# Optimization experiments

Measured on AMD Instinct MI355X. Metric: run time of the kernel, lower is better.

## Reference

```python
import jax, jax.numpy as jnp
import numpy as np

H = 16  # num_heads

def setup_inputs() -> dict:
    key = jax.random.key(0)
    k1, k2, k3, k4 = jax.random.split(key, 4)
    B, N, E = 2, 2048, 2048
    return {
        "hidden_states": jax.random.normal(k1, (B, N, E), jnp.float32),
        "w_fused": jax.random.normal(k2, (E, 3 * E), jnp.float32) * (E ** -0.5),
        "w_proj": jax.random.normal(k3, (E, E), jnp.float32) * (E ** -0.5),
        "b_proj": jax.random.normal(k4, (E,), jnp.float32),
    }

def reference(hidden_states, w_fused, w_proj, b_proj):
    B, N, E = hidden_states.shape
    D = E // H  # head_dim
    qkv = hidden_states @ w_fused                      # [B,N,3E]
    q, k, v = jnp.split(qkv, 3, axis=-1)               # each [B,N,E]
    def to_heads(t):
        return t.reshape(B, N, H, D).transpose(0, 2, 1, 3)  # [B,H,N,D]
    q, k, v = to_heads(q), to_heads(k), to_heads(v)
    scores = jnp.einsum('bhnd,bhmd->bhnm', q, k) / jnp.asarray(D ** 0.5, q.dtype)
    causal = jnp.tril(jnp.ones((N, N), dtype=bool))    # [N,N]
    mask_value = jnp.asarray(jnp.finfo(scores.dtype).min, scores.dtype)
    scores = jnp.where(causal[None, None], scores, mask_value)
    attn_weights = jax.nn.softmax(scores, axis=-1)     # [B,H,N,N]
    attn_out = jnp.einsum('bhnm,bhmd->bhnd', attn_weights, v)
    attn_out = attn_out.transpose(0, 2, 1, 3).reshape(B, N, E)  # b n (h d)
    out = attn_out @ w_proj + b_proj
    return out, attn_weights
```

## Files before the change

### kernel.cpp

```cpp
#include <hip/hip_runtime.h>
#include <hip/hip_bf16.h>

typedef __attribute__((ext_vector_type(4))) float f32x4;
typedef __attribute__((ext_vector_type(8))) __bf16 bf16x8;


__device__ inline unsigned short f2bf(float f) {
  union { float f; unsigned u; } x; x.f = f;
  unsigned r = x.u + 0x7fffu + ((x.u >> 16) & 1u);
  return (unsigned short)(r >> 16);
}

__device__ inline void stage_bf16_tile(const ushort* __restrict__ g, int ldg, ushort* l) {
  int tid = threadIdx.x;
#pragma unroll
  for (int t = 0; t < 4; ++t) {
    int c = tid + t * 256;
    int m = c >> 3, kc = (c & 7) << 3;
    *(int4*)(l + m * 72 + kc) = *(const int4*)(g + (size_t)m * ldg + kc);
  }
}

__device__ inline void stage_f32_tile(const float* __restrict__ g, int ldg, ushort* l) {
  int tid = threadIdx.x;
#pragma unroll
  for (int t = 0; t < 8; ++t) {
    int c = tid + t * 256;
    int m = c >> 4, kc = (c & 15) << 2;
    float4 v = *(const float4*)(g + (size_t)m * ldg + kc);
    ushort4 o; o.x = f2bf(v.x); o.y = f2bf(v.y); o.z = f2bf(v.z); o.w = f2bf(v.w);
    *(ushort4*)(l + m * 72 + kc) = o;
  }
}

__device__ inline void mma_tile(const ushort* lA, const ushort* lB, f32x4 acc[4][4]) {
  int lane = threadIdx.x & 63, w = threadIdx.x >> 6;
  int wm = (w & 1) << 6, wn = (w >> 1) << 6;
  int row = lane & 15, quad = lane >> 4;
#pragma unroll
  for (int kk = 0; kk < 64; kk += 32) {
    bf16x8 a[4], b[4];
#pragma unroll
    for (int i = 0; i < 4; ++i)
      a[i] = *(const bf16x8*)(lA + (wm + i * 16 + row) * 72 + kk + quad * 8);
#pragma unroll
    for (int j = 0; j < 4; ++j)
      b[j] = *(const bf16x8*)(lB + (wn + j * 16 + row) * 72 + kk + quad * 8);
#pragma unroll
    for (int i = 0; i < 4; ++i)
#pragma unroll
      for (int j = 0; j < 4; ++j)
        acc[i][j] = __builtin_amdgcn_mfma_f32_16x16x32_bf16(a[i], b[j], acc[i][j], 0, 0, 0);
  }
}


__global__ __launch_bounds__(256) void k_cvt_bf16(const float* __restrict__ in,
                                                  ushort* __restrict__ out, int n4) {
  int i = blockIdx.x * 256 + threadIdx.x;
  if (i >= n4) return;
  float4 v = *(const float4*)(in + (size_t)i * 4);
  ushort4 o; o.x = f2bf(v.x); o.y = f2bf(v.y); o.z = f2bf(v.z); o.w = f2bf(v.w);
  *(ushort4*)(out + (size_t)i * 4) = o;
}

__global__ __launch_bounds__(256) void k_transpose_bf16(const float* __restrict__ in,
                                                        ushort* __restrict__ out, int R, int C) {
  __shared__ __align__(16) ushort t[64][72];
  int c0 = blockIdx.x << 6, r0 = blockIdx.y << 6;
  int tid = threadIdx.x;
#pragma unroll
  for (int it = 0; it < 4; ++it) {
    int idx = tid + it * 256;
    int r = idx >> 4, c4 = (idx & 15) << 2;
    float4 v = *(const float4*)(in + (size_t)(r0 + r) * C + c0 + c4);
    t[c4][r] = f2bf(v.x); t[c4 + 1][r] = f2bf(v.y);
    t[c4 + 2][r] = f2bf(v.z); t[c4 + 3][r] = f2bf(v.w);
  }
  __syncthreads();
#pragma unroll
  for (int it = 0; it < 4; ++it) {
    int idx = tid + it * 256;
    int c = idx >> 4, r4 = (idx & 15) << 2;
    ushort4 o; o.x = t[c][r4]; o.y = t[c][r4 + 1]; o.z = t[c][r4 + 2]; o.w = t[c][r4 + 3];
    *(ushort4*)(out + (size_t)(c0 + c) * R + r0 + r4) = o;
  }
}

__global__ __launch_bounds__(256) void k_qkv(const ushort* __restrict__ A,
                                             const ushort* __restrict__ Bt,
                                             ushort* __restrict__ qh,
                                             ushort* __restrict__ kh,
                                             ushort* __restrict__ vt) {
  __shared__ __align__(16) ushort lA[128 * 72];
  __shared__ __align__(16) ushort lB[128 * 72];
  int rt = blockIdx.x, ct = blockIdx.y;
  f32x4 z = {0.f, 0.f, 0.f, 0.f};
  f32x4 acc[4][4];
#pragma unroll
  for (int i = 0; i < 4; ++i)
#pragma unroll
    for (int j = 0; j < 4; ++j) acc[i][j] = z;
  for (int kt = 0; kt < 2048; kt += 64) {
    __syncthreads();
    stage_bf16_tile(A + (size_t)rt * 128 * 2048 + kt, 2048, lA);
    stage_bf16_tile(Bt + (size_t)ct * 128 * 2048 + kt, 2048, lB);
    __syncthreads();
    mma_tile(lA, lB, acc);
  }
  int lane = threadIdx.x & 63, w = threadIdx.x >> 6;
  int wm = (w & 1) << 6, wn = (w >> 1) << 6;
  int col = lane & 15, rb = (lane >> 4) << 2;
#pragma unroll
  for (int i = 0; i < 4; ++i)
#pragma unroll
    for (int j = 0; j < 4; ++j)
#pragma unroll
      for (int r = 0; r < 4; ++r) {
        int R = rt * 128 + wm + i * 16 + rb + r;
        int C = ct * 128 + wn + j * 16 + col;
        int b = R >> 11, n = R & 2047;
        int seg = C >> 11, hh = (C >> 7) & 15, d = C & 127;
        int bh = b * 16 + hh;
        float v = acc[i][j][r];
        if (seg == 0)      qh[((size_t)bh * 2048 + n) * 128 + d] = f2bf(v * 0.08838834764831845f);
        else if (seg == 1) kh[((size_t)bh * 2048 + n) * 128 + d] = f2bf(v);
        else               vt[((size_t)bh * 128 + d) * 2048 + n] = f2bf(v);
      }
}

__global__ __launch_bounds__(256) void k_scores(const ushort* __restrict__ qh,
                                                const ushort* __restrict__ kh,
                                                float* __restrict__ sc) {
  int rt = blockIdx.x, ct = blockIdx.y, bh = blockIdx.z;
  if (ct > rt) return;
  __shared__ __align__(16) ushort lA[128 * 72];
  __shared__ __align__(16) ushort lB[128 * 72];
  f32x4 z = {0.f, 0.f, 0.f, 0.f};
  f32x4 acc[4][4];
#pragma unroll
  for (int i = 0; i < 4; ++i)
#pragma unroll
    for (int j = 0; j < 4; ++j) acc[i][j] = z;
  const ushort* Ab = qh + (size_t)bh * 2048 * 128 + (size_t)rt * 128 * 128;
  const ushort* Bb = kh + (size_t)bh * 2048 * 128 + (size_t)ct * 128 * 128;
#pragma unroll
  for (int kt = 0; kt < 128; kt += 64) {
    __syncthreads();
    stage_bf16_tile(Ab + kt, 128, lA);
    stage_bf16_tile(Bb + kt, 128, lB);
    __syncthreads();
    mma_tile(lA, lB, acc);
  }
  float* base = sc + (size_t)bh * 2048 * 2048;
  int lane = threadIdx.x & 63, w = threadIdx.x >> 6;
  int wm = (w & 1) << 6, wn = (w >> 1) << 6;
  int col = lane & 15, rb = (lane >> 4) << 2;
#pragma unroll
  for (int i = 0; i < 4; ++i)
#pragma unroll
    for (int j = 0; j < 4; ++j)
#pragma unroll
      for (int r = 0; r < 4; ++r) {
        int R = rt * 128 + wm + i * 16 + rb + r;
        int C = ct * 128 + wn + j * 16 + col;
        base[(size_t)R * 2048 + C] = acc[i][j][r];
      }
}

__global__ __launch_bounds__(256) void k_softmax(float* __restrict__ sc) {
  int row = blockIdx.x;
  int n = row & 2047;
  float* p = sc + (size_t)row * 2048;
  int tid = threadIdx.x;
  float vals[8];
  float mx = -INFINITY;
#pragma unroll
  for (int t = 0; t < 2; ++t) {
    float4 v = *(const float4*)(p + t * 1024 + tid * 4);
    float vv[4] = {v.x, v.y, v.z, v.w};
#pragma unroll
    for (int i = 0; i < 4; ++i) {
      int m = t * 1024 + tid * 4 + i;
      float x = (m <= n) ? vv[i] : -INFINITY;
      vals[t * 4 + i] = x;
      mx = fmaxf(mx, x);
    }
  }
#pragma unroll
  for (int o = 32; o > 0; o >>= 1) mx = fmaxf(mx, __shfl_xor(mx, o));
  __shared__ float red[4];
  if ((tid & 63) == 0) red[tid >> 6] = mx;
  __syncthreads();
  mx = fmaxf(fmaxf(red[0], red[1]), fmaxf(red[2], red[3]));
  float s = 0.f;
#pragma unroll
  for (int e = 0; e < 8; ++e) { float ev = expf(vals[e] - mx); vals[e] = ev; s += ev; }
#pragma unroll
  for (int o = 32; o > 0; o >>= 1) s += __shfl_xor(s, o);
  __syncthreads();
  if ((tid & 63) == 0) red[tid >> 6] = s;
  __syncthreads();
  float inv = 1.f / (red[0] + red[1] + red[2] + red[3]);
#pragma unroll
  for (int t = 0; t < 2; ++t) {
    float4 v;
    v.x = vals[t * 4 + 0] * inv; v.y = vals[t * 4 + 1] * inv;
    v.z = vals[t * 4 + 2] * inv; v.w = vals[t * 4 + 3] * inv;
    *(float4*)(p + t * 1024 + tid * 4) = v;
  }
}

__global__ __launch_bounds__(256) void k_pv(const float* __restrict__ sc,
                                            const ushort* __restrict__ vt,
                                            ushort* __restrict__ Ao) {
  int rt = blockIdx.x, bh = blockIdx.y;
  __shared__ __align__(16) ushort lA[128 * 72];
  __shared__ __align__(16) ushort lB[128 * 72];
  f32x4 z = {0.f, 0.f, 0.f, 0.f};
  f32x4 acc[4][4];
#pragma unroll
  for (int i = 0; i < 4; ++i)
#pragma unroll
    for (int j = 0; j < 4; ++j) acc[i][j] = z;
  const float* Pb = sc + (size_t)bh * 2048 * 2048 + (size_t)rt * 128 * 2048;
  const ushort* Vb = vt + (size_t)bh * 128 * 2048;
  int kend = (rt + 1) * 128;
  for (int kt = 0; kt < kend; kt += 64) {
    __syncthreads();
    stage_f32_tile(Pb + kt, 2048, lA);
    stage_bf16_tile(Vb + kt, 2048, lB);
    __syncthreads();
    mma_tile(lA, lB, acc);
  }
  int b = bh >> 4, hh = bh & 15;
  int lane = threadIdx.x & 63, w = threadIdx.x >> 6;
  int wm = (w & 1) << 6, wn = (w >> 1) << 6;
  int col = lane & 15, rb = (lane >> 4) << 2;
#pragma unroll
  for (int i = 0; i < 4; ++i)
#pragma unroll
    for (int j = 0; j < 4; ++j)
#pragma unroll
      for (int r = 0; r < 4; ++r) {
        int R = rt * 128 + wm + i * 16 + rb + r;
        int C = wn + j * 16 + col;
        Ao[((size_t)b * 2048 + R) * 2048 + hh * 128 + C] = f2bf(acc[i][j][r]);
      }
}

__global__ __launch_bounds__(256) void k_proj(const ushort* __restrict__ Ao,
                                              const ushort* __restrict__ Wt,
                                              const float* __restrict__ bias,
                                              float* __restrict__ out) {
  int rt = blockIdx.x, ct = blockIdx.y;
  __shared__ __align__(16) ushort lA[128 * 72];
  __shared__ __align__(16) ushort lB[128 * 72];
  f32x4 z = {0.f, 0.f, 0.f, 0.f};
  f32x4 acc[4][4];
#pragma unroll
  for (int i = 0; i < 4; ++i)
#pragma unroll
    for (int j = 0; j < 4; ++j) acc[i][j] = z;
  for (int kt = 0; kt < 2048; kt += 64) {
    __syncthreads();
    stage_bf16_tile(Ao + (size_t)rt * 128 * 2048 + kt, 2048, lA);
    stage_bf16_tile(Wt + (size_t)ct * 128 * 2048 + kt, 2048, lB);
    __syncthreads();
    mma_tile(lA, lB, acc);
  }
  int lane = threadIdx.x & 63, w = threadIdx.x >> 6;
  int wm = (w & 1) << 6, wn = (w >> 1) << 6;
  int col = lane & 15, rb = (lane >> 4) << 2;
#pragma unroll
  for (int i = 0; i < 4; ++i)
#pragma unroll
    for (int j = 0; j < 4; ++j)
#pragma unroll
      for (int r = 0; r < 4; ++r) {
        int R = rt * 128 + wm + i * 16 + rb + r;
        int C = ct * 128 + wn + j * 16 + col;
        out[(size_t)R * 2048 + C] = acc[i][j][r] + bias[C];
      }
}


extern "C" void kernel_launch(void* const* d_in, const int* in_sizes, int n_in,
                              void* d_out, int out_size, void* d_ws, size_t ws_size,
                              hipStream_t stream) {
  const float* hs = (const float*)d_in[0];
  const float* wf = (const float*)d_in[1];
  const float* wp = (const float*)d_in[2];
  const float* bp = (const float*)d_in[3];
  float* out = (float*)d_out;
  float* attnw = out + (size_t)8388608;

  ushort* Hb  = (ushort*)d_ws;
  ushort* Wft = Hb  + (size_t)8388608;
  ushort* Wpt = Wft + (size_t)12582912;
  ushort* qh  = Wpt + (size_t)4194304;
  ushort* kh  = qh  + (size_t)8388608;
  ushort* vt  = kh  + (size_t)8388608;
  ushort* Ao  = vt  + (size_t)8388608;

  k_cvt_bf16<<<8192, 256, 0, stream>>>(hs, Hb, 2097152);
  k_transpose_bf16<<<dim3(96, 32), 256, 0, stream>>>(wf, Wft, 2048, 6144);
  k_transpose_bf16<<<dim3(32, 32), 256, 0, stream>>>(wp, Wpt, 2048, 2048);
  k_qkv<<<dim3(32, 48), 256, 0, stream>>>(Hb, Wft, qh, kh, vt);
  k_scores<<<dim3(16, 16, 32), 256, 0, stream>>>(qh, kh, attnw);
  k_softmax<<<65536, 256, 0, stream>>>(attnw);
  k_pv<<<dim3(16, 32), 256, 0, stream>>>(attnw, vt, Ao);
  k_proj<<<dim3(32, 16), 256, 0, stream>>>(Ao, Wpt, bp, out);
}
```

Baseline: 1.140 ms.

## Fuse scores, softmax and PV into a two-pass causal attention kernel

Replaces the separate scores, softmax and PV kernels with one kernel per (head, row-tile). The first pass computes QK^T tiles to build the online row max and sum. The second pass recomputes the scores, writes the normalized probabilities to the attention-weights output, and multiplies them by V from LDS. The upper triangle is zero-filled directly, and row tiles are interleaved to balance the causal work. This removes the fp32 score write/read/rewrite round trips and the read of P by the PV stage, at the cost of computing QK^T twice and adding extra block-wide syncs.

```diff
diff --git a/kernel.cpp b/kernel.cpp
--- a/kernel.cpp
+++ b/kernel.cpp
@@ -21,18 +21,6 @@
   }
 }
 
-__device__ inline void stage_f32_tile(const float* __restrict__ g, int ldg, ushort* l) {
-  int tid = threadIdx.x;
-#pragma unroll
-  for (int t = 0; t < 8; ++t) {
-    int c = tid + t * 256;
-    int m = c >> 4, kc = (c & 15) << 2;
-    float4 v = *(const float4*)(g + (size_t)m * ldg + kc);
-    ushort4 o; o.x = f2bf(v.x); o.y = f2bf(v.y); o.z = f2bf(v.z); o.w = f2bf(v.w);
-    *(ushort4*)(l + m * 72 + kc) = o;
-  }
-}
-
 __device__ inline void mma_tile(const ushort* lA, const ushort* lB, f32x4 acc[4][4]) {
   int lane = threadIdx.x & 63, w = threadIdx.x >> 6;
   int wm = (w & 1) << 6, wn = (w >> 1) << 6;
@@ -46,6 +34,27 @@
 #pragma unroll
     for (int j = 0; j < 4; ++j)
       b[j] = *(const bf16x8*)(lB + (wn + j * 16 + row) * 72 + kk + quad * 8);
+#pragma unroll
+    for (int i = 0; i < 4; ++i)
+#pragma unroll
+      for (int j = 0; j < 4; ++j)
+        acc[i][j] = __builtin_amdgcn_mfma_f32_16x16x32_bf16(a[i], b[j], acc[i][j], 0, 0, 0);
+  }
+}
+
+__device__ inline void mma_pv(const ushort* lP, const ushort* lV, int kk2, f32x4 acc[4][4]) {
+  int lane = threadIdx.x & 63, w = threadIdx.x >> 6;
+  int wm = (w & 1) << 6, wn = (w >> 1) << 6;
+  int row = lane & 15, quad = lane >> 4;
+#pragma unroll
+  for (int kk = 0; kk < 64; kk += 32) {
+    bf16x8 a[4], b[4];
+#pragma unroll
+    for (int i = 0; i < 4; ++i)
+      a[i] = *(const bf16x8*)(lP + (wm + i * 16 + row) * 136 + kk2 * 64 + kk + quad * 8);
+#pragma unroll
+    for (int j = 0; j < 4; ++j)
+      b[j] = *(const bf16x8*)(lV + (wn + j * 16 + row) * 72 + kk + quad * 8);
 #pragma unroll
     for (int i = 0; i < 4; ++i)
 #pragma unroll
@@ -129,123 +138,169 @@
       }
 }
 
-__global__ __launch_bounds__(256) void k_scores(const ushort* __restrict__ qh,
-                                                const ushort* __restrict__ kh,
-                                                float* __restrict__ sc) {
-  int rt = blockIdx.x, ct = blockIdx.y, bh = blockIdx.z;
-  if (ct > rt) return;
-  __shared__ __align__(16) ushort lA[128 * 72];
-  __shared__ __align__(16) ushort lB[128 * 72];
+__global__ __launch_bounds__(256, 2) void k_attn(const ushort* __restrict__ qh,
+                                                 const ushort* __restrict__ kh,
+                                                 const ushort* __restrict__ vt,
+                                                 float* __restrict__ attnw,
+                                                 ushort* __restrict__ Ao) {
+  __shared__ __align__(16) ushort lAB[2 * 128 * 72];
+  __shared__ __align__(16) ushort lV[128 * 72];
+  __shared__ float mArr[128], lArr[128], invA[128], tm0[128], tm1[128];
+
+  int id = blockIdx.x;
+  int r5 = id & 31, p = r5 >> 1;
+  int rt = (r5 & 1) ? p : 15 - p;
+  int bh = ((id >> 5) << 1) | ((id >> 4) & 1);
+
+  ushort* lA = lAB;
+  ushort* lB = lAB + 128 * 72;
+  int tid = threadIdx.x;
+  int lane = tid & 63, w = tid >> 6;
+  int wm = (w & 1) << 6, wn = (w >> 1) << 6;
+  int c16 = lane & 15, quad = lane >> 4;
+
+  const ushort* Qb = qh + ((size_t)bh * 2048 + rt * 128) * 128;
+  const ushort* Kb = kh + (size_t)bh * 2048 * 128;
+  const ushort* Vb = vt + (size_t)bh * 128 * 2048;
+  float* Pg = attnw + (size_t)bh * 2048 * 2048 + (size_t)rt * 128 * 2048;
+
+  if (tid < 128) { mArr[tid] = -INFINITY; lArr[tid] = 0.f; }
+  __syncthreads();
+
   f32x4 z = {0.f, 0.f, 0.f, 0.f};
-  f32x4 acc[4][4];
-#pragma unroll
-  for (int i = 0; i < 4; ++i)
-#pragma unroll
-    for (int j = 0; j < 4; ++j) acc[i][j] = z;
-  const ushort* Ab = qh + (size_t)bh * 2048 * 128 + (size_t)rt * 128 * 128;
-  const ushort* Bb = kh + (size_t)bh * 2048 * 128 + (size_t)ct * 128 * 128;
-#pragma unroll
-  for (int kt = 0; kt < 128; kt += 64) {
-    __syncthreads();
-    stage_bf16_tile(Ab + kt, 128, lA);
-    stage_bf16_tile(Bb + kt, 128, lB);
-    __syncthreads();
-    mma_tile(lA, lB, acc);
-  }
-  float* base = sc + (size_t)bh * 2048 * 2048;
-  int lane = threadIdx.x & 63, w = threadIdx.x >> 6;
-  int wm = (w & 1) << 6, wn = (w >> 1) << 6;
-  int col = lane & 15, rb = (lane >> 4) << 2;
-#pragma unroll
-  for (int i = 0; i < 4; ++i)
-#pragma unroll
-    for (int j = 0; j < 4; ++j)
-#pragma unroll
-      for (int r = 0; r < 4; ++r) {
-        int R = rt * 128 + wm + i * 16 + rb + r;
-        int C = ct * 128 + wn + j * 16 + col;
-        base[(size_t)R * 2048 + C] = acc[i][j][r];
-      }
-}
-
-__global__ __launch_bounds__(256) void k_softmax(float* __restrict__ sc) {
-  int row = blockIdx.x;
-  int n = row & 2047;
-  float* p = sc + (size_t)row * 2048;
-  int tid = threadIdx.x;
-  float vals[8];
-  float mx = -INFINITY;
-#pragma unroll
-  for (int t = 0; t < 2; ++t) {
-    float4 v = *(const float4*)(p + t * 1024 + tid * 4);
-    float vv[4] = {v.x, v.y, v.z, v.w};
-#pragma unroll
-    for (int i = 0; i < 4; ++i) {
-      int m = t * 1024 + tid * 4 + i;
-      float x = (m <= n) ? vv[i] : -INFINITY;
-      vals[t * 4 + i] = x;
-      mx = fmaxf(mx, x);
+  float* tmw = (wn == 0) ? tm0 : tm1;
+
+  for (int ct = 0; ct <= rt; ++ct) {
+    f32x4 acc[4][4];
+#pragma unroll
+    for (int i = 0; i < 4; ++i)
+#pragma unroll
+      for (int j = 0; j < 4; ++j) acc[i][j] = z;
+#pragma unroll
+    for (int kt = 0; kt < 128; kt += 64) {
+      __syncthreads();
+      stage_bf16_tile(Qb + kt, 128, lA);
+      stage_bf16_tile(Kb + (size_t)ct * 128 * 128 + kt, 128, lB);
+      __syncthreads();
+      mma_tile(lA, lB, acc);
     }
-  }
-#pragma unroll
-  for (int o = 32; o > 0; o >>= 1) mx = fmaxf(mx, __shfl_xor(mx, o));
-  __shared__ float red[4];
-  if ((tid & 63) == 0) red[tid >> 6] = mx;
+    bool diag = (ct == rt);
+#pragma unroll
+    for (int i = 0; i < 4; ++i)
+#pragma unroll
+      for (int r = 0; r < 4; ++r) {
+        int lr = wm + i * 16 + quad * 4 + r;
+        float mx = -INFINITY;
+#pragma unroll
+        for (int j = 0; j < 4; ++j) {
+          int lc = wn + j * 16 + c16;
+          if (!diag || lc <= lr) mx = fmaxf(mx, acc[i][j][r]);
+        }
+#pragma unroll
+        for (int o = 1; o < 16; o <<= 1) mx = fmaxf(mx, __shfl_xor(mx, o));
+        if (c16 == 0) tmw[lr] = mx;
+      }
+    __syncthreads();
+    if (tid < 128) {
+      float tmax = fmaxf(tm0[tid], tm1[tid]);
+      float mo = mArr[tid];
+      float mn = fmaxf(mo, tmax);
+      float corr = (mo == -INFINITY) ? 0.f : __expf(mo - mn);
+      mArr[tid] = mn;
+      lArr[tid] *= corr;
+    }
+    __syncthreads();
+#pragma unroll
+    for (int i = 0; i < 4; ++i)
+#pragma unroll
+      for (int r = 0; r < 4; ++r) {
+        int lr = wm + i * 16 + quad * 4 + r;
+        float mn = mArr[lr];
+        float s = 0.f;
+#pragma unroll
+        for (int j = 0; j < 4; ++j) {
+          int lc = wn + j * 16 + c16;
+          if (!diag || lc <= lr) s += __expf(acc[i][j][r] - mn);
+        }
+#pragma unroll
+        for (int o = 1; o < 16; o <<= 1) s += __shfl_xor(s, o);
+        if (c16 == 0) tmw[lr] = s;
+      }
+    __syncthreads();
+    if (tid < 128) lArr[tid] += tm0[tid] + tm1[tid];
+  }
   __syncthreads();
-  mx = fmaxf(fmaxf(red[0], red[1]), fmaxf(red[2], red[3]));
-  float s = 0.f;
-#pragma unroll
-  for (int e = 0; e < 8; ++e) { float ev = expf(vals[e] - mx); vals[e] = ev; s += ev; }
-#pragma unroll
-  for (int o = 32; o > 0; o >>= 1) s += __shfl_xor(s, o);
+  if (tid < 128) invA[tid] = 1.f / lArr[tid];
   __syncthreads();
-  if ((tid & 63) == 0) red[tid >> 6] = s;
-  __syncthreads();
-  float inv = 1.f / (red[0] + red[1] + red[2] + red[3]);
-#pragma unroll
-  for (int t = 0; t < 2; ++t) {
-    float4 v;
-    v.x = vals[t * 4 + 0] * inv; v.y = vals[t * 4 + 1] * inv;
-    v.z = vals[t * 4 + 2] * inv; v.w = vals[t * 4 + 3] * inv;
-    *(float4*)(p + t * 1024 + tid * 4) = v;
-  }
-}
-
-__global__ __launch_bounds__(256) void k_pv(const float* __restrict__ sc,
-                                            const ushort* __restrict__ vt,
-                                            ushort* __restrict__ Ao) {
-  int rt = blockIdx.x, bh = blockIdx.y;
-  __shared__ __align__(16) ushort lA[128 * 72];
-  __shared__ __align__(16) ushort lB[128 * 72];
-  f32x4 z = {0.f, 0.f, 0.f, 0.f};
-  f32x4 acc[4][4];
-#pragma unroll
-  for (int i = 0; i < 4; ++i)
-#pragma unroll
-    for (int j = 0; j < 4; ++j) acc[i][j] = z;
-  const float* Pb = sc + (size_t)bh * 2048 * 2048 + (size_t)rt * 128 * 2048;
-  const ushort* Vb = vt + (size_t)bh * 128 * 2048;
-  int kend = (rt + 1) * 128;
-  for (int kt = 0; kt < kend; kt += 64) {
-    __syncthreads();
-    stage_f32_tile(Pb + kt, 2048, lA);
-    stage_bf16_tile(Vb + kt, 2048, lB);
-    __syncthreads();
-    mma_tile(lA, lB, acc);
-  }
+
+  f32x4 o2[4][4];
+#pragma unroll
+  for (int i = 0; i < 4; ++i)
+#pragma unroll
+    for (int j = 0; j < 4; ++j) o2[i][j] = z;
+
+  for (int ct = 0; ct <= rt; ++ct) {
+    f32x4 acc[4][4];
+#pragma unroll
+    for (int i = 0; i < 4; ++i)
+#pragma unroll
+      for (int j = 0; j < 4; ++j) acc[i][j] = z;
+#pragma unroll
+    for (int kt = 0; kt < 128; kt += 64) {
+      __syncthreads();
+      stage_bf16_tile(Qb + kt, 128, lA);
+      stage_bf16_tile(Kb + (size_t)ct * 128 * 128 + kt, 128, lB);
+      __syncthreads();
+      mma_tile(lA, lB, acc);
+    }
+    __syncthreads();
+    bool diag = (ct == rt);
+    ushort* lP = lAB;
+#pragma unroll
+    for (int i = 0; i < 4; ++i)
+#pragma unroll
+      for (int r = 0; r < 4; ++r) {
+        int lr = wm + i * 16 + quad * 4 + r;
+        float mn = mArr[lr], inv = invA[lr];
+        float* prow = Pg + (size_t)lr * 2048 + ct * 128;
+#pragma unroll
+        for (int j = 0; j < 4; ++j) {
+          int lc = wn + j * 16 + c16;
+          float e = (!diag || lc <= lr) ? __expf(acc[i][j][r] - mn) * inv : 0.f;
+          lP[lr * 136 + lc] = f2bf(e);
+          prow[lc] = e;
+        }
+      }
+    stage_bf16_tile(Vb + ct * 128, 2048, lV);
+    __syncthreads();
+    mma_pv(lP, lV, 0, o2);
+    __syncthreads();
+    stage_bf16_tile(Vb + ct * 128 + 64, 2048, lV);
+    __syncthreads();
+    mma_pv(lP, lV, 1, o2);
+  }
+
+  float4 z4 = make_float4(0.f, 0.f, 0.f, 0.f);
+  for (int ct = rt + 1; ct < 16; ++ct) {
+    float* T = Pg + ct * 128;
+#pragma unroll
+    for (int it = 0; it < 16; ++it) {
+      int idx = tid + it * 256;
+      int rr = idx >> 5, cc = (idx & 31) << 2;
+      *(float4*)(T + (size_t)rr * 2048 + cc) = z4;
+    }
+  }
+
   int b = bh >> 4, hh = bh & 15;
-  int lane = threadIdx.x & 63, w = threadIdx.x >> 6;
-  int wm = (w & 1) << 6, wn = (w >> 1) << 6;
-  int col = lane & 15, rb = (lane >> 4) << 2;
-#pragma unroll
-  for (int i = 0; i < 4; ++i)
-#pragma unroll
-    for (int j = 0; j < 4; ++j)
-#pragma unroll
-      for (int r = 0; r < 4; ++r) {
-        int R = rt * 128 + wm + i * 16 + rb + r;
-        int C = wn + j * 16 + col;
-        Ao[((size_t)b * 2048 + R) * 2048 + hh * 128 + C] = f2bf(acc[i][j][r]);
+#pragma unroll
+  for (int i = 0; i < 4; ++i)
+#pragma unroll
+    for (int j = 0; j < 4; ++j)
+#pragma unroll
+      for (int r = 0; r < 4; ++r) {
+        int R = rt * 128 + wm + i * 16 + quad * 4 + r;
+        int C = wn + j * 16 + c16;
+        Ao[((size_t)b * 2048 + R) * 2048 + hh * 128 + C] = f2bf(o2[i][j][r]);
       }
 }
 
@@ -307,8 +362,6 @@
   k_transpose_bf16<<<dim3(96, 32), 256, 0, stream>>>(wf, Wft, 2048, 6144);
   k_transpose_bf16<<<dim3(32, 32), 256, 0, stream>>>(wp, Wpt, 2048, 2048);
   k_qkv<<<dim3(32, 48), 256, 0, stream>>>(Hb, Wft, qh, kh, vt);
-  k_scores<<<dim3(16, 16, 32), 256, 0, stream>>>(qh, kh, attnw);
-  k_softmax<<<65536, 256, 0, stream>>>(attnw);
-  k_pv<<<dim3(16, 32), 256, 0, stream>>>(attnw, vt, Ao);
+  k_attn<<<512, 256, 0, stream>>>(qh, kh, vt, attnw, Ao);
   k_proj<<<dim3(32, 16), 256, 0, stream>>>(Ao, Wpt, bp, out);
 }
```

After: 1.130 ms. Within noise of the previous version (-0.9%).
